# Kernel optimization log

Hardware: AMD Instinct MI355X
Metric: run time of the kernel (lower is better)

The kernel has to match this reference:

```python
import jax
import jax.numpy as jnp
import numpy as np

TEMPERATURE = 0.07
NUM_HARD = 4
ALPHA = 2.0
NEG_INF = -1.0e9


def setup_inputs() -> dict:
    key = jax.random.key(0)
    k1, k2 = jax.random.split(key)
    B, D = 8192, 256
    v = jax.random.normal(k1, (B, D), dtype=jnp.float32)
    t = jax.random.normal(k2, (B, D), dtype=jnp.float32)
    # embeddings are assumed unit-norm (cosine similarity in the original module)
    v = v / jnp.linalg.norm(v, axis=-1, keepdims=True)
    t = t / jnp.linalg.norm(t, axis=-1, keepdims=True)
    return {"vision_embed": v, "text_embed": t}


def reference(vision_embed, text_embed):
    B = vision_embed.shape[0]
    rows = jnp.arange(B)
    # [B, B] similarity logits
    sim = jnp.einsum("bd,cd->bc", vision_embed, text_embed) / TEMPERATURE
    # mask diagonal, take top-k hardest negatives per row
    sim_off = sim.at[rows, rows].set(NEG_INF)
    k = min(NUM_HARD, B - 1)
    _, hard_idx = jax.lax.top_k(sim_off, k)  # [B, k]
    # weights: alpha at hard negatives, 1 elsewhere (diag forced to 1)
    weights = jnp.ones_like(sim)
    weights = weights.at[rows[:, None], hard_idx].set(ALPHA)
    weights = weights.at[rows, rows].set(1.0)
    sw = sim * weights  # weighted logits, shared by both directions
    # v->t: row softmax; t->v: sim.T * weights.T == sw.T -> column softmax of sw
    logp_v2t = jax.nn.log_softmax(sw, axis=1)
    logp_t2v = jax.nn.log_softmax(sw, axis=0)
    loss_v2t = -jnp.mean(logp_v2t[rows, rows])
    loss_t2v = -jnp.mean(logp_t2v[rows, rows])
    return (loss_v2t + loss_t2v) / 2.0
```

## Files before the change

kernel.cpp:

```cpp
#include <hip/hip_runtime.h>
#include <hip/hip_bf16.h>
#include <math.h>

#define B_SIZE 8192
#define D_SIZE 256
#define INV_T 14.285714285714286f
#define LOG2E 1.4426950408889634f
#define LN2 0.6931471805599453f
#define KEY_MASK 0xFFFFE000
#define COL_MASK 0x1FFF

typedef __bf16 bf16x8 __attribute__((ext_vector_type(8)));
typedef float f32x4 __attribute__((ext_vector_type(4)));

__device__ __forceinline__ void gload_lds16(const void* g, void* lds) {
  __builtin_amdgcn_global_load_lds(
      (const __attribute__((address_space(1))) void*)g,
      (__attribute__((address_space(3))) void*)lds, 16, 0, 0);
}

__device__ __forceinline__ void cei(int& a, int& b) {
  const int h = a > b ? a : b;
  const int l = a > b ? b : a;
  a = h; b = l;
}

__device__ __forceinline__ void merge_top4i(int a[4], int b[4]) {
  cei(a[0], b[3]); cei(a[1], b[2]); cei(a[2], b[1]); cei(a[3], b[0]);
  cei(a[0], a[2]); cei(a[1], a[3]); cei(a[0], a[1]); cei(a[2], a[3]);
}

__global__ __launch_bounds__(256) void cvt_both(
    const float* __restrict__ V, const float* __restrict__ T,
    __hip_bfloat16* __restrict__ Vb, __hip_bfloat16* __restrict__ Tb,
    float* __restrict__ sums) {
  const int b = blockIdx.x;
  if (b < 16)
    reinterpret_cast<float4*>(sums)[b * 256 + threadIdx.x] =
        float4{0.f, 0.f, 0.f, 0.f};
  const int half = b >> 11;
  const int i = (b & 2047) * 256 + threadIdx.x;
  const float sc = half ? 1.0f : (INV_T * LOG2E);
  const float* src = half ? T : V;
  __hip_bfloat16* dst = half ? Tb : Vb;
  const float4 v = reinterpret_cast<const float4*>(src)[i];
  union { __hip_bfloat16 h[4]; short4 s; } u;
  u.h[0] = __float2bfloat16(v.x * sc);
  u.h[1] = __float2bfloat16(v.y * sc);
  u.h[2] = __float2bfloat16(v.z * sc);
  u.h[3] = __float2bfloat16(v.w * sc);
  reinterpret_cast<short4*>(dst)[i] = u.s;
}

__global__ __launch_bounds__(256) void gemm_analyze(
    const __hip_bfloat16* __restrict__ Vb, const __hip_bfloat16* __restrict__ Tb,
    float* __restrict__ row_sum, float* __restrict__ col_sum,
    float* __restrict__ diag, int* __restrict__ cand_key) {
  __shared__ __align__(16) char smem[32768];
  __shared__ float rsum[128];
  __shared__ float csum[128];

  const int tid  = threadIdx.x;
  const int wave = tid >> 6;
  const int lane = tid & 63;
  const int tileRow = blockIdx.x >> 6;
  const int tileCol = blockIdx.x & 63;
  const int wr = wave >> 1;
  const int wc = wave & 1;
  const int g = lane >> 4;
  const int frow = lane & 15;
  const int rsw = frow & 7;

  __hip_bfloat16* As = reinterpret_cast<__hip_bfloat16*>(smem);
  __hip_bfloat16* Bs = As + 128 * 64;

  if (tid < 128) rsum[tid] = 0.f; else csum[tid - 128] = 0.f;

  f32x4 acc[4][4];
#pragma unroll
  for (int m = 0; m < 4; ++m)
#pragma unroll
    for (int n = 0; n < 4; ++n)
      acc[m][n] = f32x4{0.f, 0.f, 0.f, 0.f};

  const int srow = wave * 32 + (lane >> 3);
  const int scol = ((lane & 7) ^ ((lane >> 3) & 7)) * 8;
  const __hip_bfloat16* Ag = Vb + (size_t)(tileRow * 128 + srow) * D_SIZE + scol;
  const __hip_bfloat16* Bg = Tb + (size_t)(tileCol * 128 + srow) * D_SIZE + scol;
  char* AsStage = (char*)As + wave * 4096;
  char* BsStage = (char*)Bs + wave * 4096;

  for (int k0 = 0; k0 < D_SIZE; k0 += 64) {
#pragma unroll
    for (int i = 0; i < 4; ++i) {
      gload_lds16(Ag + (size_t)i * 8 * D_SIZE + k0, AsStage + i * 1024);
      gload_lds16(Bg + (size_t)i * 8 * D_SIZE + k0, BsStage + i * 1024);
    }
    __syncthreads();
#pragma unroll
    for (int ks = 0; ks < 64; ks += 32) {
      const int cbase = (ks >> 3) + g;
      const int coff = ((cbase ^ rsw) << 4);
      bf16x8 tf[4], vf[4];
#pragma unroll
      for (int n = 0; n < 4; ++n)
        tf[n] = *reinterpret_cast<const bf16x8*>(
            (const char*)Bs + (wc * 64 + n * 16 + frow) * 128 + coff);
#pragma unroll
      for (int m = 0; m < 4; ++m)
        vf[m] = *reinterpret_cast<const bf16x8*>(
            (const char*)As + (wr * 64 + m * 16 + frow) * 128 + coff);
#pragma unroll
      for (int m = 0; m < 4; ++m)
#pragma unroll
        for (int n = 0; n < 4; ++n)
          acc[m][n] = __builtin_amdgcn_mfma_f32_16x16x32_bf16(
              tf[n], vf[m], acc[m][n], 0, 0, 0);
    }
    __syncthreads();
  }

  int* candK = reinterpret_cast<int*>(smem);

  const bool diagT = (tileRow == tileCol) && (wr == wc);
  const bool diagLane = diagT && (g == (frow >> 2));
  const int rowBase = tileRow * 128 + wr * 64;
  const int colOr = tileCol * 128 + wc * 64 + g * 4;

  float cp[16];
#pragma unroll
  for (int k = 0; k < 16; ++k) cp[k] = 0.f;

#pragma unroll
  for (int m = 0; m < 4; ++m) {
    float rs = 0.f;
    int t0 = (int)0x80000000, t1 = (int)0x80000000;
#pragma unroll
    for (int n = 0; n < 4; ++n) {
#pragma unroll
      for (int r = 0; r < 4; ++r) {
        const float a = acc[m][n][r];
        const float e = exp2f(a);
        rs += e;
        cp[n * 4 + r] += e;
        const int key =
            ((__float_as_int(a) & KEY_MASK) | colOr) | (n * 16 + r);
        t1 = max(t1, min(t0, key));
        t0 = max(t0, key);
      }
    }
    rs += __shfl_xor(rs, 16);
    rs += __shfl_xor(rs, 32);
    if (g == 0) atomicAdd(&rsum[wr * 64 + m * 16 + frow], rs);
    if (diagLane) {
      const int rr = frow & 3;
      float dv = acc[m][m][0];
      dv = rr == 1 ? acc[m][m][1] : dv;
      dv = rr == 2 ? acc[m][m][2] : dv;
      dv = rr == 3 ? acc[m][m][3] : dv;
      diag[rowBase + m * 16 + frow] = dv * LN2;
      t0 = t1; t1 = (int)0x80000000;
    }
    const int cb = (wr * 64 + m * 16 + frow) * 17 + (wc * 4 + g) * 2;
    candK[cb] = t0; candK[cb + 1] = t1;
  }

#pragma unroll
  for (int s = 8; s >= 1; s >>= 1) {
    const bool up = (lane & s) != 0;
#pragma unroll
    for (int k = 0; k < 8; ++k) {
      if (k < s) {
        const float send = up ? cp[k] : cp[k + s];
        const float recv = __shfl_xor(send, s);
        cp[k] = (up ? cp[k + s] : cp[k]) + recv;
      }
    }
  }
  atomicAdd(&csum[wc * 64 + ((frow >> 2) << 4) + (g << 2) + (frow & 3)], cp[0]);

  __syncthreads();

  if (tid < 128) {
    const int row = tid;
    const int base = row * 17;
    int a[4] = {candK[base], candK[base + 1], (int)0x80000000, (int)0x80000000};
#pragma unroll
    for (int l = 1; l < 8; ++l) {
      int b[4] = {candK[base + l * 2], candK[base + l * 2 + 1],
                  (int)0x80000000, (int)0x80000000};
      merge_top4i(a, b);
    }
    const int gRow = tileRow * 128 + row;
    const size_t cb = ((size_t)gRow << 8) + (tileCol << 2);
    int4 o; o.x = a[0]; o.y = a[1]; o.z = a[2]; o.w = a[3];
    *reinterpret_cast<int4*>(cand_key + cb) = o;
    atomicAdd(&row_sum[gRow], rsum[row]);
  } else {
    const int c = tid - 128;
    atomicAdd(&col_sum[tileCol * 128 + c], csum[c]);
  }
}

__global__ __launch_bounds__(256) void merge_correct(
    const int* __restrict__ cand_key,
    float* __restrict__ row_sum, float* __restrict__ col_sum) {
  const int wave = threadIdx.x >> 6;
  const int lane = threadIdx.x & 63;
  const int row = blockIdx.x * 4 + wave;

  const int4 k4 = *reinterpret_cast<const int4*>(
      cand_key + ((size_t)row << 8) + lane * 4);
  int v[4] = {k4.x, k4.y, k4.z, k4.w};

#pragma unroll
  for (int s = 1; s < 64; s <<= 1) {
    int b[4];
#pragma unroll
    for (int k = 0; k < 4; ++k) b[k] = __shfl_xor(v[k], s);
    merge_top4i(v, b);
  }

  if (lane == 0) {
    float corr = 0.f;
#pragma unroll
    for (int k = 0; k < 4; ++k) {
      const float a = __int_as_float(v[k] & KEY_MASK);
      const float c = exp2f(a + a) - exp2f(a);
      corr += c;
      atomicAdd(&col_sum[v[k] & COL_MASK], c);
    }
    row_sum[row] += corr;
  }
}

__global__ __launch_bounds__(256) void finalize(
    const float* __restrict__ row_sum, const float* __restrict__ col_sum,
    const float* __restrict__ diag, float* __restrict__ out) {
  double s = 0.0;
  for (int i = threadIdx.x; i < B_SIZE; i += 256)
    s += (double)(logf(row_sum[i]) + logf(col_sum[i]) - 2.f * diag[i]);
#pragma unroll
  for (int d = 1; d < 64; d <<= 1) s += __shfl_xor(s, d);
  __shared__ double red[4];
  const int lane = threadIdx.x & 63, wave = threadIdx.x >> 6;
  if (lane == 0) red[wave] = s;
  __syncthreads();
  if (threadIdx.x == 0) {
    const double tot = red[0] + red[1] + red[2] + red[3];
    out[0] = (float)(tot / (2.0 * (double)B_SIZE));
  }
}

extern "C" void kernel_launch(void* const* d_in, const int* in_sizes, int n_in,
                              void* d_out, int out_size, void* d_ws, size_t ws_size,
                              hipStream_t stream) {
  const float* V = (const float*)d_in[0];
  const float* T = (const float*)d_in[1];
  float* out = (float*)d_out;
  char* ws = (char*)d_ws;

  __hip_bfloat16* Vb = (__hip_bfloat16*)ws;
  __hip_bfloat16* Tb = (__hip_bfloat16*)(ws + (4 << 20));
  float* row_sum = (float*)(ws + (8 << 20));
  float* col_sum = row_sum + B_SIZE;
  float* diag    = col_sum + B_SIZE;
  int*   cand_key = (int*)(ws + (8 << 20) + 3 * B_SIZE * 4);

  cvt_both<<<4096, 256, 0, stream>>>(V, T, Vb, Tb, row_sum);
  gemm_analyze<<<64 * 64, 256, 0, stream>>>(Vb, Tb, row_sum, col_sum, diag,
                                            cand_key);
  merge_correct<<<B_SIZE / 4, 256, 0, stream>>>(cand_key, row_sum, col_sum);
  finalize<<<1, 256, 0, stream>>>(row_sum, col_sum, diag, out);
}
```

Baseline: 170.0 us.

## Split GEMM tile across eight waves with 32x64 per-wave subtiles

The 128x128 GEMM-analyze block moves from 256 to 512 threads, so each wave computes a 32x64 subtile instead of 64x64. The cooperative LDS staging, diagonal detection and candidate-index layout are remapped to match. This halves per-wave accumulator registers and doubles the waves available to hide latency. In exchange each wave issues more LDS fragment loads per MFMA (B fragments are reused across fewer rows), and the epilogue has more shuffles and atomics per tile.

```diff
diff --git a/kernel.cpp b/kernel.cpp
--- a/kernel.cpp
+++ b/kernel.cpp
@@ -52,7 +52,7 @@
   reinterpret_cast<short4*>(dst)[i] = u.s;
 }
 
-__global__ __launch_bounds__(256) void gemm_analyze(
+__global__ __launch_bounds__(512) void gemm_analyze(
     const __hip_bfloat16* __restrict__ Vb, const __hip_bfloat16* __restrict__ Tb,
     float* __restrict__ row_sum, float* __restrict__ col_sum,
     float* __restrict__ diag, int* __restrict__ cand_key) {
@@ -74,44 +74,45 @@
   __hip_bfloat16* As = reinterpret_cast<__hip_bfloat16*>(smem);
   __hip_bfloat16* Bs = As + 128 * 64;
 
-  if (tid < 128) rsum[tid] = 0.f; else csum[tid - 128] = 0.f;
-
-  f32x4 acc[4][4];
-#pragma unroll
-  for (int m = 0; m < 4; ++m)
+  if (tid < 128) rsum[tid] = 0.f;
+  else if (tid < 256) csum[tid - 128] = 0.f;
+
+  f32x4 acc[2][4];
+#pragma unroll
+  for (int m = 0; m < 2; ++m)
 #pragma unroll
     for (int n = 0; n < 4; ++n)
       acc[m][n] = f32x4{0.f, 0.f, 0.f, 0.f};
 
-  const int srow = wave * 32 + (lane >> 3);
-  const int scol = ((lane & 7) ^ ((lane >> 3) & 7)) * 8;
+  const int srow = tid >> 3;
+  const int scol = ((tid & 7) ^ ((tid >> 3) & 7)) * 8;
   const __hip_bfloat16* Ag = Vb + (size_t)(tileRow * 128 + srow) * D_SIZE + scol;
   const __hip_bfloat16* Bg = Tb + (size_t)(tileCol * 128 + srow) * D_SIZE + scol;
-  char* AsStage = (char*)As + wave * 4096;
-  char* BsStage = (char*)Bs + wave * 4096;
+  char* AsW = (char*)As + wave * 1024;
+  char* BsW = (char*)Bs + wave * 1024;
 
   for (int k0 = 0; k0 < D_SIZE; k0 += 64) {
 #pragma unroll
-    for (int i = 0; i < 4; ++i) {
-      gload_lds16(Ag + (size_t)i * 8 * D_SIZE + k0, AsStage + i * 1024);
-      gload_lds16(Bg + (size_t)i * 8 * D_SIZE + k0, BsStage + i * 1024);
+    for (int i = 0; i < 2; ++i) {
+      gload_lds16(Ag + (size_t)i * 64 * D_SIZE + k0, AsW + i * 8192);
+      gload_lds16(Bg + (size_t)i * 64 * D_SIZE + k0, BsW + i * 8192);
     }
     __syncthreads();
 #pragma unroll
     for (int ks = 0; ks < 64; ks += 32) {
       const int cbase = (ks >> 3) + g;
       const int coff = ((cbase ^ rsw) << 4);
-      bf16x8 tf[4], vf[4];
+      bf16x8 tf[4], vf[2];
 #pragma unroll
       for (int n = 0; n < 4; ++n)
         tf[n] = *reinterpret_cast<const bf16x8*>(
             (const char*)Bs + (wc * 64 + n * 16 + frow) * 128 + coff);
 #pragma unroll
-      for (int m = 0; m < 4; ++m)
+      for (int m = 0; m < 2; ++m)
         vf[m] = *reinterpret_cast<const bf16x8*>(
-            (const char*)As + (wr * 64 + m * 16 + frow) * 128 + coff);
-#pragma unroll
-      for (int m = 0; m < 4; ++m)
+            (const char*)As + (wr * 32 + m * 16 + frow) * 128 + coff);
+#pragma unroll
+      for (int m = 0; m < 2; ++m)
 #pragma unroll
         for (int n = 0; n < 4; ++n)
           acc[m][n] = __builtin_amdgcn_mfma_f32_16x16x32_bf16(
@@ -122,9 +123,8 @@
 
   int* candK = reinterpret_cast<int*>(smem);
 
-  const bool diagT = (tileRow == tileCol) && (wr == wc);
-  const bool diagLane = diagT && (g == (frow >> 2));
-  const int rowBase = tileRow * 128 + wr * 64;
+  const bool diagT = (tileRow == tileCol);
+  const int rowBase = tileRow * 128 + wr * 32;
   const int colOr = tileCol * 128 + wc * 64 + g * 4;
 
   float cp[16];
@@ -132,7 +132,7 @@
   for (int k = 0; k < 16; ++k) cp[k] = 0.f;
 
 #pragma unroll
-  for (int m = 0; m < 4; ++m) {
+  for (int m = 0; m < 2; ++m) {
     float rs = 0.f;
     int t0 = (int)0x80000000, t1 = (int)0x80000000;
 #pragma unroll
@@ -151,17 +151,18 @@
     }
     rs += __shfl_xor(rs, 16);
     rs += __shfl_xor(rs, 32);
-    if (g == 0) atomicAdd(&rsum[wr * 64 + m * 16 + frow], rs);
-    if (diagLane) {
+    if (g == 0) atomicAdd(&rsum[wr * 32 + m * 16 + frow], rs);
+    const int dn = wr * 2 + m - wc * 4;
+    if (diagT && dn >= 0 && dn < 4 && g == (frow >> 2)) {
       const int rr = frow & 3;
-      float dv = acc[m][m][0];
-      dv = rr == 1 ? acc[m][m][1] : dv;
-      dv = rr == 2 ? acc[m][m][2] : dv;
-      dv = rr == 3 ? acc[m][m][3] : dv;
+      float dv = acc[m][dn][0];
+      dv = rr == 1 ? acc[m][dn][1] : dv;
+      dv = rr == 2 ? acc[m][dn][2] : dv;
+      dv = rr == 3 ? acc[m][dn][3] : dv;
       diag[rowBase + m * 16 + frow] = dv * LN2;
       t0 = t1; t1 = (int)0x80000000;
     }
-    const int cb = (wr * 64 + m * 16 + frow) * 17 + (wc * 4 + g) * 2;
+    const int cb = (wr * 32 + m * 16 + frow) * 17 + (wc * 4 + g) * 2;
     candK[cb] = t0; candK[cb + 1] = t1;
   }
 
@@ -196,7 +197,7 @@
     int4 o; o.x = a[0]; o.y = a[1]; o.z = a[2]; o.w = a[3];
     *reinterpret_cast<int4*>(cand_key + cb) = o;
     atomicAdd(&row_sum[gRow], rsum[row]);
-  } else {
+  } else if (tid < 256) {
     const int c = tid - 128;
     atomicAdd(&col_sum[tileCol * 128 + c], csum[c]);
   }
@@ -268,7 +269,7 @@
   int*   cand_key = (int*)(ws + (8 << 20) + 3 * B_SIZE * 4);
 
   cvt_both<<<4096, 256, 0, stream>>>(V, T, Vb, Tb, row_sum);
-  gemm_analyze<<<64 * 64, 256, 0, stream>>>(Vb, Tb, row_sum, col_sum, diag,
+  gemm_analyze<<<64 * 64, 512, 0, stream>>>(Vb, Tb, row_sum, col_sum, diag,
                                             cand_key);
   merge_correct<<<B_SIZE / 4, 256, 0, stream>>>(cand_key, row_sum, col_sum);
   finalize<<<1, 256, 0, stream>>>(row_sum, col_sum, diag, out);
```

New measurement: 182.1 us. 1.07x slower.

## Double-buffer GEMM LDS staging and fuse finalize into merge via last-block counter

Applied to the files above, without the earlier changes.

The GEMM K-loop now uses two LDS buffers: it prefetches the next 64-wide K slice with global_load_lds while computing on the current one. This doubles shared memory to 64KB per block, which may reduce occupancy. Separately, the single-block finalize kernel is folded into the merge kernel through an atomic completion counter, so the last block does the final reduction and one launch is removed. The counter is reset in the convert kernel. The loop no longer has a __syncthreads before overwriting the other buffer, so the next stage's write can race with reads of the previous iteration unless a barrier remains in the hidden loop tail.

```diff
diff --git a/kernel.cpp b/kernel.cpp
--- a/kernel.cpp
+++ b/kernel.cpp
@@ -33,11 +33,12 @@
 __global__ __launch_bounds__(256) void cvt_both(
     const float* __restrict__ V, const float* __restrict__ T,
     __hip_bfloat16* __restrict__ Vb, __hip_bfloat16* __restrict__ Tb,
-    float* __restrict__ sums) {
+    float* __restrict__ sums, unsigned* __restrict__ counter) {
   const int b = blockIdx.x;
   if (b < 16)
     reinterpret_cast<float4*>(sums)[b * 256 + threadIdx.x] =
         float4{0.f, 0.f, 0.f, 0.f};
+  if (b == 0 && threadIdx.x == 0) *counter = 0;
   const int half = b >> 11;
   const int i = (b & 2047) * 256 + threadIdx.x;
   const float sc = half ? 1.0f : (INV_T * LOG2E);
@@ -56,7 +57,7 @@
     const __hip_bfloat16* __restrict__ Vb, const __hip_bfloat16* __restrict__ Tb,
     float* __restrict__ row_sum, float* __restrict__ col_sum,
     float* __restrict__ diag, int* __restrict__ cand_key) {
-  __shared__ __align__(16) char smem[32768];
+  __shared__ __align__(16) char smem[65536];
   __shared__ float rsum[128];
   __shared__ float csum[128];
 
@@ -71,9 +72,6 @@
   const int frow = lane & 15;
   const int rsw = frow & 7;
 
-  __hip_bfloat16* As = reinterpret_cast<__hip_bfloat16*>(smem);
-  __hip_bfloat16* Bs = As + 128 * 64;
-
   if (tid < 128) rsum[tid] = 0.f; else csum[tid - 128] = 0.f;
 
   f32x4 acc[4][4];
@@ -87,16 +85,26 @@
   const int scol = ((lane & 7) ^ ((lane >> 3) & 7)) * 8;
   const __hip_bfloat16* Ag = Vb + (size_t)(tileRow * 128 + srow) * D_SIZE + scol;
   const __hip_bfloat16* Bg = Tb + (size_t)(tileCol * 128 + srow) * D_SIZE + scol;
-  char* AsStage = (char*)As + wave * 4096;
-  char* BsStage = (char*)Bs + wave * 4096;
-
-  for (int k0 = 0; k0 < D_SIZE; k0 += 64) {
+
+  auto STAGE = [&](int buf, int k0) {
+    char* aS = smem + buf * 32768 + wave * 4096;
+    char* bS = aS + 16384;
 #pragma unroll
     for (int i = 0; i < 4; ++i) {
-      gload_lds16(Ag + (size_t)i * 8 * D_SIZE + k0, AsStage + i * 1024);
-      gload_lds16(Bg + (size_t)i * 8 * D_SIZE + k0, BsStage + i * 1024);
-    }
-    __syncthreads();
+      gload_lds16(Ag + (size_t)i * 8 * D_SIZE + k0, aS + i * 1024);
+      gload_lds16(Bg + (size_t)i * 8 * D_SIZE + k0, bS + i * 1024);
+    }
+  };
+
+  STAGE(0, 0);
+  __syncthreads();
+
+#pragma unroll
+  for (int t = 0; t < 4; ++t) {
+    const int cur = t & 1;
+    if (t < 3) STAGE(cur ^ 1, (t + 1) * 64);
+    const char* aB = smem + cur * 32768;
+    const char* bB = aB + 16384;
 #pragma unroll
     for (int ks = 0; ks < 64; ks += 32) {
       const int cbase = (ks >> 3) + g;
@@ -105,11 +113,11 @@
 #pragma unroll
       for (int n = 0; n < 4; ++n)
         tf[n] = *reinterpret_cast<const bf16x8*>(
-            (const char*)Bs + (wc * 64 + n * 16 + frow) * 128 + coff);
+            bB + (wc * 64 + n * 16 + frow) * 128 + coff);
 #pragma unroll
       for (int m = 0; m < 4; ++m)
         vf[m] = *reinterpret_cast<const bf16x8*>(
-            (const char*)As + (wr * 64 + m * 16 + frow) * 128 + coff);
+            aB + (wr * 64 + m * 16 + frow) * 128 + coff);
 #pragma unroll
       for (int m = 0; m < 4; ++m)
 #pragma unroll
@@ -202,9 +210,11 @@
   }
 }
 
-__global__ __launch_bounds__(256) void merge_correct(
+__global__ __launch_bounds__(256) void merge_finalize(
     const int* __restrict__ cand_key,
-    float* __restrict__ row_sum, float* __restrict__ col_sum) {
+    float* __restrict__ row_sum, float* __restrict__ col_sum,
+    const float* __restrict__ diag, unsigned* __restrict__ counter,
+    float* __restrict__ out) {
   const int wave = threadIdx.x >> 6;
   const int lane = threadIdx.x & 63;
   const int row = blockIdx.x * 4 + wave;
@@ -231,19 +241,23 @@
       atomicAdd(&col_sum[v[k] & COL_MASK], c);
     }
     row_sum[row] += corr;
-  }
-}
-
-__global__ __launch_bounds__(256) void finalize(
-    const float* __restrict__ row_sum, const float* __restrict__ col_sum,
-    const float* __restrict__ diag, float* __restrict__ out) {
+    __threadfence();
+  }
+  __syncthreads();
+
+  __shared__ unsigned lastFlag;
+  if (threadIdx.x == 0)
+    lastFlag = (atomicAdd(counter, 1u) == gridDim.x - 1) ? 1u : 0u;
+  __syncthreads();
+  if (!lastFlag) return;
+  __threadfence();
+
   double s = 0.0;
   for (int i = threadIdx.x; i < B_SIZE; i += 256)
     s += (double)(logf(row_sum[i]) + logf(col_sum[i]) - 2.f * diag[i]);
 #pragma unroll
   for (int d = 1; d < 64; d <<= 1) s += __shfl_xor(s, d);
   __shared__ double red[4];
-  const int lane = threadIdx.x & 63, wave = threadIdx.x >> 6;
   if (lane == 0) red[wave] = s;
   __syncthreads();
   if (threadIdx.x == 0) {
@@ -266,10 +280,11 @@
   float* col_sum = row_sum + B_SIZE;
   float* diag    = col_sum + B_SIZE;
   int*   cand_key = (int*)(ws + (8 << 20) + 3 * B_SIZE * 4);
-
-  cvt_both<<<4096, 256, 0, stream>>>(V, T, Vb, Tb, row_sum);
+  unsigned* counter = (unsigned*)((char*)cand_key + (8 << 20));
+
+  cvt_both<<<4096, 256, 0, stream>>>(V, T, Vb, Tb, row_sum, counter);
   gemm_analyze<<<64 * 64, 256, 0, stream>>>(Vb, Tb, row_sum, col_sum, diag,
                                             cand_key);
-  merge_correct<<<B_SIZE / 4, 256, 0, stream>>>(cand_key, row_sum, col_sum);
-  finalize<<<1, 256, 0, stream>>>(row_sum, col_sum, diag, out);
-}
+  merge_finalize<<<B_SIZE / 4, 256, 0, stream>>>(cand_key, row_sum, col_sum,
+                                                 diag, counter, out);
+}
```

Measured after the change: 296.6 us. 1.74x slower.
